# Optimization experiments

Hardware: AMD Instinct MI355X
Metric: run time of the kernel (lower is better)

## Reference

```python
import jax, jax.numpy as jnp
import numpy as np

B, S, OUT = 128, 3000, 84
CODE_SEQ = 30
LAT = 1024
C, D = 128, 16
CB = C * D  # 2048
IN = CODE_SEQ * OUT  # 2520


def setup_inputs() -> dict:
    key = jax.random.key(0)
    ks = jax.random.split(key, 16)
    def w(k, shape):
        fan_in = shape[0]
        return (jax.random.normal(k, shape, dtype=jnp.float32) / np.sqrt(fan_in)).astype(jnp.float32)
    return {
        "y": jax.random.normal(ks[0], (B, S, OUT), dtype=jnp.float32),
        "emb": jax.random.uniform(ks[1], (C, D), minval=-1.0 / C, maxval=1.0 / C, dtype=jnp.float32),
        "eW1": w(ks[2], (IN, LAT)), "eb1": jnp.zeros((LAT,), jnp.float32),
        "eW2": w(ks[3], (LAT, LAT)), "eb2": jnp.zeros((LAT,), jnp.float32),
        "eW3": w(ks[4], (LAT, CB)), "eb3": jnp.zeros((CB,), jnp.float32),
        "dW1": w(ks[5], (CB, LAT)), "db1": jnp.zeros((LAT,), jnp.float32),
        "dW2": w(ks[6], (LAT, LAT)), "db2": jnp.zeros((LAT,), jnp.float32),
        "dW3": w(ks[7], (LAT, IN)), "db3": jnp.zeros((IN,), jnp.float32),
    }


def _mlp(z, W1, b1, W2, b2, W3, b3):
    # LinearEncoder in eval mode (dropout = identity): Linear->ELU->Linear->ELU->Linear
    z = jax.nn.elu(z @ W1 + b1)
    z = jax.nn.elu(z @ W2 + b2)
    return z @ W3 + b3


def reference(y, emb, eW1, eb1, eW2, eb2, eW3, eb3, dW1, db1, dW2, db2, dW3, db3):
    batch, seq_len = y.shape[0], y.shape[1]
    # seq_len % code_seq == 0 -> padding branch is a no-op
    y2 = y.reshape(batch, -1, IN)                 # (B, n_m, 2520)
    n_m = y2.shape[1]
    ze = _mlp(y2, eW1, eb1, eW2, eb2, eW3, eb3)   # (B, n_m, 2048)
    zef = ze.reshape(batch, n_m, -1, D)           # (B, n_m, G=128, 16)
    # squared L2 distance to each of C codes, without materializing (B,n_m,G,C,D)
    dist = (
        jnp.sum(zef ** 2, -1, keepdims=True)
        - 2.0 * jnp.einsum("bngd,cd->bngc", zef, emb)
        + jnp.sum(emb ** 2, -1)
    )                                             # (B, n_m, G, C)
    nn_idx = jnp.argmin(dist, -1)                 # (B, n_m, G)
    zq = emb[nn_idx].reshape(batch, n_m, -1)      # (B, n_m, 2048)
    dec_in = ze + jax.lax.stop_gradient(zq - ze)  # straight-through
    out = _mlp(dec_in, dW1, db1, dW2, db2, dW3, db3)
    out = out.reshape(batch, -1, OUT)[:, :seq_len, :]
    return (out, ze, zq)
```

## Files before the change

kernel.cpp:

```cpp
#include <hip/hip_runtime.h>
#include <hip/hip_bf16.h>
#include <cstdint>
#include <cstddef>

typedef __bf16 bf16_t;
typedef bf16_t bf16x8 __attribute__((ext_vector_type(8)));
typedef float  f32x4  __attribute__((ext_vector_type(4)));

__device__ __forceinline__ void gl_lds16(const void* g, void* l) {
  __builtin_amdgcn_global_load_lds(
      (const __attribute__((address_space(1))) void*)g,
      (__attribute__((address_space(3))) void*)l, 16, 0, 0);
}

#define BAR()  __builtin_amdgcn_s_barrier()
#define LGK0() asm volatile("s_waitcnt lgkmcnt(0)" ::: "memory")

__device__ __forceinline__ void transpose_tile(
    const float* __restrict__ W, bf16_t* __restrict__ Wt,
    int K, int N, int Kpad, int Npad, int bx, int by, int t)
{
  __shared__ float tile[32][33];
  const int tx = t & 31, ty = t >> 5;
  const int k0 = bx * 32, n0 = by * 32;
#pragma unroll
  for (int i = 0; i < 4; ++i) {
    int k = k0 + ty + i * 8, n = n0 + tx;
    tile[ty + i * 8][tx] = (k < K && n < N) ? W[(size_t)k * N + n] : 0.f;
  }
  __syncthreads();
#pragma unroll
  for (int i = 0; i < 4; ++i) {
    int n = n0 + ty + i * 8, k = k0 + tx;
    if (n < Npad && k < Kpad)
      Wt[(size_t)n * Kpad + k] = (bf16_t)tile[tx][ty + i * 8];
  }
}

__global__ __launch_bounds__(256) void prep_kernel(
    const float* __restrict__ y, bf16_t* __restrict__ X0,
    const float* __restrict__ eW1, bf16_t* __restrict__ W1t,
    const float* __restrict__ eW2, bf16_t* __restrict__ W2t,
    const float* __restrict__ eW3, bf16_t* __restrict__ W3t,
    const float* __restrict__ dW1, bf16_t* __restrict__ V1t,
    const float* __restrict__ dW2, bf16_t* __restrict__ V2t,
    const float* __restrict__ dW3, bf16_t* __restrict__ V3t)
{
  const int b = blockIdx.x;
  const int t = threadIdx.x;
  if (b < 16000) {
    const int idx = b * 256 + t;
    const int r = idx / 320, c = (idx % 320) * 8;
    bf16x8 v;
    if (c < 2520) {
      const float4 f0 = *(const float4*)(y + (size_t)r * 2520 + c);
      const float4 f1 = *(const float4*)(y + (size_t)r * 2520 + c + 4);
      v[0] = (bf16_t)f0.x; v[1] = (bf16_t)f0.y; v[2] = (bf16_t)f0.z; v[3] = (bf16_t)f0.w;
      v[4] = (bf16_t)f1.x; v[5] = (bf16_t)f1.y; v[6] = (bf16_t)f1.z; v[7] = (bf16_t)f1.w;
    } else {
#pragma unroll
      for (int j = 0; j < 8; ++j) v[j] = (bf16_t)0.f;
    }
    *(bf16x8*)(X0 + (size_t)r * 2560 + c) = v;
    return;
  }
  int lb = b - 16000;
  if (lb < 2560)      { transpose_tile(eW1, W1t, 2520, 1024, 2560, 1024, lb % 80, lb / 80, t); return; }
  lb -= 2560;
  if (lb < 1024)      { transpose_tile(eW2, W2t, 1024, 1024, 1024, 1024, lb % 32, lb / 32, t); return; }
  lb -= 1024;
  if (lb < 2048)      { transpose_tile(eW3, W3t, 1024, 2048, 1024, 2048, lb % 32, lb / 32, t); return; }
  lb -= 2048;
  if (lb < 2048)      { transpose_tile(dW1, V1t, 2048, 1024, 2048, 1024, lb % 64, lb / 64, t); return; }
  lb -= 2048;
  if (lb < 1024)      { transpose_tile(dW2, V2t, 1024, 1024, 1024, 1024, lb % 32, lb / 32, t); return; }
  lb -= 1024;
  transpose_tile(dW3, V3t, 1024, 2520, 1024, 2560, lb % 32, lb / 32, t);
}

template<int ELU>
__global__ __launch_bounds__(512, 2) void gemm256(
    const bf16_t* __restrict__ A, const bf16_t* __restrict__ Bt,
    const float* __restrict__ bias,
    bf16_t* __restrict__ Cb, float* __restrict__ Cf,
    int M, int N, int K, int Nlog)
{
  __shared__ __align__(16) bf16_t lds[65536];

  const int t  = threadIdx.x;
  const int w  = t >> 6, l = t & 63;
  const int fr = l & 15, kg = l >> 4;
  const int wm = (w >> 2) * 128, wn = (w & 3) * 64;

  const int gx = gridDim.x;
  const int nwg = gx * (int)gridDim.y;
  int lin = blockIdx.y * gx + blockIdx.x;
  int q8 = nwg >> 3, r8 = nwg & 7, xcd = lin & 7, idx = lin >> 3;
  int swz = (xcd < r8 ? xcd * (q8 + 1) : r8 * (q8 + 1) + (xcd - r8) * q8) + idx;
  const int tn = (swz % gx) * 256;
  const int tm = (swz / gx) * 256;

  const int srow = t >> 2;
  const int scol = (t & 3) * 8;
  const int sdst = t * 8;

  const int NT = K >> 5;

  f32x4 acc[8][4];
#pragma unroll
  for (int i = 0; i < 8; ++i)
#pragma unroll
    for (int j = 0; j < 4; ++j) acc[i][j] = (f32x4){0.f, 0.f, 0.f, 0.f};

  auto stageA = [&](int slot, int kn) {
    bf16_t* d = lds + slot * 16384;
    gl_lds16(A + (size_t)(tm + srow) * K + kn + scol,       d + sdst);
    gl_lds16(A + (size_t)(tm + 128 + srow) * K + kn + scol, d + 4096 + sdst);
  };
  auto stageB = [&](int slot, int kn) {
    bf16_t* d = lds + slot * 16384 + 8192;
    gl_lds16(Bt + (size_t)(tn + srow) * K + kn + scol,       d + sdst);
    gl_lds16(Bt + (size_t)(tn + 128 + srow) * K + kn + scol, d + 4096 + sdst);
  };

  stageA(0, 0);  stageB(0, 0);
  stageA(1, 32); stageB(1, 32);
  stageA(2, 64); stageB(2, 64);
  asm volatile("s_waitcnt vmcnt(8)" ::: "memory");
  BAR();

  for (int kt = 0; kt < NT; ++kt) {
    const int slot = kt & 3;
    const bf16_t* aH = lds + slot * 16384 + wm * 32;
    const bf16_t* bH = lds + slot * 16384 + 8192 + wn * 32;
    const bool pf = (kt + 3 < NT);
    const int ps = (kt + 3) & 3;
    const int kn = (kt + 3) << 5;

    bf16x8 af[8], bf_[2];

#pragma unroll
    for (int mi = 0; mi < 8; ++mi)
      af[mi] = *(const bf16x8*)(aH + (mi * 16 + fr) * 32 + kg * 8);
#pragma unroll
    for (int nj = 0; nj < 2; ++nj)
      bf_[nj] = *(const bf16x8*)(bH + (nj * 16 + fr) * 32 + kg * 8);
    if (pf) stageA(ps, kn);
    BAR(); LGK0();
    __builtin_amdgcn_s_setprio(1);
#pragma unroll
    for (int mi = 0; mi < 8; ++mi)
#pragma unroll
      for (int nj = 0; nj < 2; ++nj)
        acc[mi][nj] = __builtin_amdgcn_mfma_f32_16x16x32_bf16(af[mi], bf_[nj], acc[mi][nj], 0, 0, 0);
    __builtin_amdgcn_s_setprio(0);
    BAR();

#pragma unroll
    for (int nj = 0; nj < 2; ++nj)
      bf_[nj] = *(const bf16x8*)(bH + ((nj + 2) * 16 + fr) * 32 + kg * 8);
    if (pf) stageB(ps, kn);
    BAR(); LGK0();
    __builtin_amdgcn_s_setprio(1);
#pragma unroll
    for (int mi = 0; mi < 8; ++mi)
#pragma unroll
      for (int nj = 0; nj < 2; ++nj)
        acc[mi][nj + 2] = __builtin_amdgcn_mfma_f32_16x16x32_bf16(af[mi], bf_[nj], acc[mi][nj + 2], 0, 0, 0);
    __builtin_amdgcn_s_setprio(0);
    asm volatile("s_waitcnt vmcnt(8)" ::: "memory");
    BAR();
  }

#pragma unroll
  for (int mi = 0; mi < 8; ++mi) {
    const int row0 = tm + wm + mi * 16 + kg * 4;
#pragma unroll
    for (int nj = 0; nj < 4; ++nj) {
      const int col = tn + wn + nj * 16 + fr;
      const float bv = (col < Nlog) ? bias[col] : 0.f;
#pragma unroll
      for (int r = 0; r < 4; ++r) {
        float v = acc[mi][nj][r] + bv;
        if (ELU) v = (v > 0.f) ? v : expm1f(v);
        const int row = row0 + r;
        if (Cb) Cb[(size_t)row * N + col] = (bf16_t)v;
        if (Cf && col < Nlog) Cf[(size_t)row * Nlog + col] = v;
      }
    }
  }
}

__global__ __launch_bounds__(256) void vq_mfma(
    const float* __restrict__ ze, const float* __restrict__ emb,
    float* __restrict__ zq, bf16_t* __restrict__ zqb)
{
  __shared__ float  se[2048];
  __shared__ bf16_t seb[2048];
  const int t = threadIdx.x;
  for (int i = t; i < 2048; i += 256) { float v = emb[i]; se[i] = v; seb[i] = (bf16_t)v; }
  __syncthreads();

  const int l = t & 63, w = t >> 6;
  const int col = l & 15;
  const int ks8 = (l >> 4) * 8;
  const bool kact = (ks8 < 16);

  bf16x8 bfrag[8];
  float  hv[8];
#pragma unroll
  for (int cb = 0; cb < 8; ++cb) {
    float s = 0.f;
    bf16x8 bf;
#pragma unroll
    for (int j = 0; j < 8; ++j) bf[j] = (bf16_t)0.f;
    if (kact) {
      const float* ep = se + (cb * 16 + col) * 16 + ks8;
      float4 e0 = *(const float4*)ep;
      float4 e1 = *(const float4*)(ep + 4);
      bf[0] = (bf16_t)e0.x; bf[1] = (bf16_t)e0.y; bf[2] = (bf16_t)e0.z; bf[3] = (bf16_t)e0.w;
      bf[4] = (bf16_t)e1.x; bf[5] = (bf16_t)e1.y; bf[6] = (bf16_t)e1.z; bf[7] = (bf16_t)e1.w;
      s = e0.x*e0.x + e0.y*e0.y + e0.z*e0.z + e0.w*e0.w
        + e1.x*e1.x + e1.y*e1.y + e1.z*e1.z + e1.w*e1.w;
    }
    s += __shfl_xor(s, 16);
    s += __shfl_xor(s, 32);
    bfrag[cb] = bf;
    hv[cb] = 0.5f * s;
  }

  const int base_tile = blockIdx.x * 64 + w * 16;
  for (int it = 0; it < 16; ++it) {
    const int tile = base_tile + it;
    const int row = tile >> 3, g0 = (tile & 7) * 16;

    bf16x8 afrag;
#pragma unroll
    for (int j = 0; j < 8; ++j) afrag[j] = (bf16_t)0.f;
    if (kact) {
      const float* ap = ze + (size_t)row * 2048 + (g0 + col) * 16 + ks8;
      float4 a0 = *(const float4*)ap;
      float4 a1 = *(const float4*)(ap + 4);
      afrag[0] = (bf16_t)(-a0.x); afrag[1] = (bf16_t)(-a0.y);
      afrag[2] = (bf16_t)(-a0.z); afrag[3] = (bf16_t)(-a0.w);
      afrag[4] = (bf16_t)(-a1.x); afrag[5] = (bf16_t)(-a1.y);
      afrag[6] = (bf16_t)(-a1.z); afrag[7] = (bf16_t)(-a1.w);
    }

    f32x4 dd[8];
#pragma unroll
    for (int cb = 0; cb < 8; ++cb) {
      f32x4 c = (f32x4){hv[cb], hv[cb], hv[cb], hv[cb]};
      dd[cb] = __builtin_amdgcn_mfma_f32_16x16x32_bf16(afrag, bfrag[cb], c, 0, 0, 0);
    }

#pragma unroll
    for (int r = 0; r < 4; ++r) {
      float bd = dd[0][r]; int bi = col;
#pragma unroll
      for (int cb = 1; cb < 8; ++cb) {
        float v = dd[cb][r];
        int   ci = cb * 16 + col;
        if (v < bd) { bd = v; bi = ci; }
      }
#pragma unroll
      for (int m = 1; m < 16; m <<= 1) {
        float od = __shfl_xor(bd, m);
        int   oi = __shfl_xor(bi, m);
        if (od < bd || (od == bd && oi < bi)) { bd = od; bi = oi; }
      }
      if (col == r) {
        const int tok = (l >> 4) * 4 + r;
        const size_t go = ((size_t)row * 128 + g0 + tok) * 16;
        const float*  e  = se  + bi * 16;
        const bf16_t* eb = seb + bi * 16;
#pragma unroll
        for (int v = 0; v < 4; ++v)
          *(float4*)(zq + go + v * 4) = ((const float4*)e)[v];
        *(bf16x8*)(zqb + go)     = ((const bf16x8*)eb)[0];
        *(bf16x8*)(zqb + go + 8) = ((const bf16x8*)eb)[1];
      }
    }
  }
}

extern "C" void kernel_launch(void* const* d_in, const int* in_sizes, int n_in,
                              void* d_out, int out_size, void* d_ws, size_t ws_size,
                              hipStream_t stream)
{
  const float* y   = (const float*)d_in[0];
  const float* emb = (const float*)d_in[1];
  const float* eW1 = (const float*)d_in[2];
  const float* eb1 = (const float*)d_in[3];
  const float* eW2 = (const float*)d_in[4];
  const float* eb2 = (const float*)d_in[5];
  const float* eW3 = (const float*)d_in[6];
  const float* eb3 = (const float*)d_in[7];
  const float* dW1 = (const float*)d_in[8];
  const float* db1 = (const float*)d_in[9];
  const float* dW2 = (const float*)d_in[10];
  const float* db2 = (const float*)d_in[11];
  const float* dW3 = (const float*)d_in[12];
  const float* db3 = (const float*)d_in[13];

  float* out = (float*)d_out;
  float* ze  = out + 32256000;
  float* zq  = ze + 26214400;

  uint8_t* ws = (uint8_t*)d_ws;
  size_t off = 0;
  auto alloc = [&](size_t bytes) -> void* {
    void* p = ws + off; off += (bytes + 255) & ~(size_t)255; return p;
  };
  bf16_t* X0  = (bf16_t*)alloc(12800ULL * 2560 * 2);
  bf16_t* W1t = (bf16_t*)alloc(1024ULL * 2560 * 2);
  bf16_t* W2t = (bf16_t*)alloc(1024ULL * 1024 * 2);
  bf16_t* W3t = (bf16_t*)alloc(2048ULL * 1024 * 2);
  bf16_t* V1t = (bf16_t*)alloc(1024ULL * 2048 * 2);
  bf16_t* V2t = (bf16_t*)alloc(1024ULL * 1024 * 2);
  bf16_t* V3t = (bf16_t*)alloc(2560ULL * 1024 * 2);
  bf16_t* H1  = (bf16_t*)alloc(12800ULL * 1024 * 2);
  bf16_t* H2  = (bf16_t*)alloc(12800ULL * 1024 * 2);
  bf16_t* ZQb = (bf16_t*)alloc(12800ULL * 2048 * 2);

  prep_kernel<<<27264, 256, 0, stream>>>(y, X0, eW1, W1t, eW2, W2t, eW3, W3t,
                                         dW1, V1t, dW2, V2t, dW3, V3t);

  gemm256<1><<<dim3(4, 50), 512, 0, stream>>>(X0, W1t, eb1, H1, nullptr, 12800, 1024, 2560, 1024);
  gemm256<1><<<dim3(4, 50), 512, 0, stream>>>(H1, W2t, eb2, H2, nullptr, 12800, 1024, 1024, 1024);
  gemm256<0><<<dim3(8, 50), 512, 0, stream>>>(H2, W3t, eb3, nullptr, ze, 12800, 2048, 1024, 2048);
  vq_mfma<<<1600, 256, 0, stream>>>(ze, emb, zq, ZQb);
  gemm256<1><<<dim3(4, 50), 512, 0, stream>>>(ZQb, V1t, db1, H1, nullptr, 12800, 1024, 2048, 1024);
  gemm256<1><<<dim3(4, 50), 512, 0, stream>>>(H1, V2t, db2, H2, nullptr, 12800, 1024, 1024, 1024);
  gemm256<0><<<dim3(10, 50), 512, 0, stream>>>(H2, V3t, db3, nullptr, out, 12800, 2560, 1024, 2520);
}
```

Before: 662.5 us.

## Fuse all MLP GEMMs and VQ into persistent kernel with dataflow flags

Replaces the six GEMM launches and the VQ launch with one persistent kernel of 256 workgroups. Each workgroup pulls work items from a global atomic counter and waits on per-row-block completion counters before running a tile. This lets later layers start on finished row blocks while earlier layers are still running, removing launch gaps and the idle tail of each 200-tile layer. The cost is atomic polling and spin-waits, two extra hidden-activation buffers, and a dependence on every workgroup being resident at once to avoid deadlock.

```diff
diff --git a/kernel.cpp b/kernel.cpp
--- a/kernel.cpp
+++ b/kernel.cpp
@@ -44,10 +44,14 @@
     const float* __restrict__ eW3, bf16_t* __restrict__ W3t,
     const float* __restrict__ dW1, bf16_t* __restrict__ V1t,
     const float* __restrict__ dW2, bf16_t* __restrict__ V2t,
-    const float* __restrict__ dW3, bf16_t* __restrict__ V3t)
+    const float* __restrict__ dW3, bf16_t* __restrict__ V3t,
+    int* __restrict__ flags)
 {
   const int b = blockIdx.x;
   const int t = threadIdx.x;
+  if (b == 0) {
+    for (int i = t; i < 512; i += 256) flags[i] = 0;
+  }
   if (b < 16000) {
     const int idx = b * 256 + t;
     const int r = idx / 320, c = (idx % 320) * 8;
@@ -78,208 +82,254 @@
   transpose_tile(dW3, V3t, 1024, 2520, 1024, 2560, lb % 32, lb / 32, t);
 }
 
-template<int ELU>
-__global__ __launch_bounds__(512, 2) void gemm256(
-    const bf16_t* __restrict__ A, const bf16_t* __restrict__ Bt,
-    const float* __restrict__ bias,
-    bf16_t* __restrict__ Cb, float* __restrict__ Cf,
-    int M, int N, int K, int Nlog)
+__global__ __launch_bounds__(512, 2) void mega_kernel(
+    const bf16_t* __restrict__ X0,
+    const bf16_t* __restrict__ W1t, const bf16_t* __restrict__ W2t,
+    const bf16_t* __restrict__ W3t, const bf16_t* __restrict__ V1t,
+    const bf16_t* __restrict__ V2t, const bf16_t* __restrict__ V3t,
+    const float* __restrict__ eb1, const float* __restrict__ eb2,
+    const float* __restrict__ eb3, const float* __restrict__ db1,
+    const float* __restrict__ db2, const float* __restrict__ db3,
+    bf16_t* __restrict__ H1, bf16_t* __restrict__ H2,
+    bf16_t* __restrict__ H3, bf16_t* __restrict__ H4,
+    bf16_t* __restrict__ ZQb,
+    float* __restrict__ ze, float* __restrict__ zq, float* __restrict__ outp,
+    const float* __restrict__ emb, int* __restrict__ flags)
 {
-  __shared__ __align__(16) bf16_t lds[65536];
-
-  const int t  = threadIdx.x;
-  const int w  = t >> 6, l = t & 63;
+  __shared__ __align__(16) char smem[131072];
+  __shared__ int s_idx;
+  bf16_t* lds = (bf16_t*)smem;
+
+  const int t = threadIdx.x;
+  const int w = t >> 6, l = t & 63;
   const int fr = l & 15, kg = l >> 4;
-  const int wm = (w >> 2) * 128, wn = (w & 3) * 64;
-
-  const int gx = gridDim.x;
-  const int nwg = gx * (int)gridDim.y;
-  int lin = blockIdx.y * gx + blockIdx.x;
-  int q8 = nwg >> 3, r8 = nwg & 7, xcd = lin & 7, idx = lin >> 3;
-  int swz = (xcd < r8 ? xcd * (q8 + 1) : r8 * (q8 + 1) + (xcd - r8) * q8) + idx;
-  const int tn = (swz % gx) * 256;
-  const int tm = (swz / gx) * 256;
-
-  const int srow = t >> 2;
-  const int scol = (t & 3) * 8;
-  const int sdst = t * 8;
-
-  const int NT = K >> 5;
-
-  f32x4 acc[8][4];
-#pragma unroll
-  for (int i = 0; i < 8; ++i)
-#pragma unroll
-    for (int j = 0; j < 4; ++j) acc[i][j] = (f32x4){0.f, 0.f, 0.f, 0.f};
-
-  auto stageA = [&](int slot, int kn) {
-    bf16_t* d = lds + slot * 16384;
-    gl_lds16(A + (size_t)(tm + srow) * K + kn + scol,       d + sdst);
-    gl_lds16(A + (size_t)(tm + 128 + srow) * K + kn + scol, d + 4096 + sdst);
-  };
-  auto stageB = [&](int slot, int kn) {
-    bf16_t* d = lds + slot * 16384 + 8192;
-    gl_lds16(Bt + (size_t)(tn + srow) * K + kn + scol,       d + sdst);
-    gl_lds16(Bt + (size_t)(tn + 128 + srow) * K + kn + scol, d + 4096 + sdst);
-  };
-
-  stageA(0, 0);  stageB(0, 0);
-  stageA(1, 32); stageB(1, 32);
-  stageA(2, 64); stageB(2, 64);
-  asm volatile("s_waitcnt vmcnt(8)" ::: "memory");
-  BAR();
-
-  for (int kt = 0; kt < NT; ++kt) {
-    const int slot = kt & 3;
-    const bf16_t* aH = lds + slot * 16384 + wm * 32;
-    const bf16_t* bH = lds + slot * 16384 + 8192 + wn * 32;
-    const bool pf = (kt + 3 < NT);
-    const int ps = (kt + 3) & 3;
-    const int kn = (kt + 3) << 5;
-
-    bf16x8 af[8], bf_[2];
-
-#pragma unroll
-    for (int mi = 0; mi < 8; ++mi)
-      af[mi] = *(const bf16x8*)(aH + (mi * 16 + fr) * 32 + kg * 8);
-#pragma unroll
-    for (int nj = 0; nj < 2; ++nj)
-      bf_[nj] = *(const bf16x8*)(bH + (nj * 16 + fr) * 32 + kg * 8);
-    if (pf) stageA(ps, kn);
-    BAR(); LGK0();
-    __builtin_amdgcn_s_setprio(1);
-#pragma unroll
-    for (int mi = 0; mi < 8; ++mi)
-#pragma unroll
-      for (int nj = 0; nj < 2; ++nj)
-        acc[mi][nj] = __builtin_amdgcn_mfma_f32_16x16x32_bf16(af[mi], bf_[nj], acc[mi][nj], 0, 0, 0);
-    __builtin_amdgcn_s_setprio(0);
-    BAR();
-
-#pragma unroll
-    for (int nj = 0; nj < 2; ++nj)
-      bf_[nj] = *(const bf16x8*)(bH + ((nj + 2) * 16 + fr) * 32 + kg * 8);
-    if (pf) stageB(ps, kn);
-    BAR(); LGK0();
-    __builtin_amdgcn_s_setprio(1);
-#pragma unroll
-    for (int mi = 0; mi < 8; ++mi)
-#pragma unroll
-      for (int nj = 0; nj < 2; ++nj)
-        acc[mi][nj + 2] = __builtin_amdgcn_mfma_f32_16x16x32_bf16(af[mi], bf_[nj], acc[mi][nj + 2], 0, 0, 0);
-    __builtin_amdgcn_s_setprio(0);
-    asm volatile("s_waitcnt vmcnt(8)" ::: "memory");
-    BAR();
-  }
-
-#pragma unroll
-  for (int mi = 0; mi < 8; ++mi) {
-    const int row0 = tm + wm + mi * 16 + kg * 4;
-#pragma unroll
-    for (int nj = 0; nj < 4; ++nj) {
-      const int col = tn + wn + nj * 16 + fr;
-      const float bv = (col < Nlog) ? bias[col] : 0.f;
-#pragma unroll
-      for (int r = 0; r < 4; ++r) {
-        float v = acc[mi][nj][r] + bv;
-        if (ELU) v = (v > 0.f) ? v : expm1f(v);
-        const int row = row0 + r;
-        if (Cb) Cb[(size_t)row * N + col] = (bf16_t)v;
-        if (Cf && col < Nlog) Cf[(size_t)row * Nlog + col] = v;
-      }
+
+  for (;;) {
+    if (t == 0)
+      s_idx = __hip_atomic_fetch_add(&flags[0], 1, __ATOMIC_RELAXED, __HIP_MEMORY_SCOPE_AGENT);
+    __syncthreads();
+    const int idx = s_idx;
+    if (idx >= 1900) break;
+
+    int layer, m, n = 0, i = idx;
+    if      (i < 200)  { layer = 0;            m = i >> 2; n = i & 3; }
+    else if (i < 400)  { layer = 1; i -= 200;  m = i >> 2; n = i & 3; }
+    else if (i < 800)  { layer = 2; i -= 400;  m = i >> 3; n = i & 7; }
+    else if (i < 1000) { layer = 3; i -= 800;  m = i; }
+    else if (i < 1200) { layer = 4; i -= 1000; m = i >> 2; n = i & 3; }
+    else if (i < 1400) { layer = 5; i -= 1200; m = i >> 2; n = i & 3; }
+    else               { layer = 6; i -= 1400; m = i / 10; n = i % 10; }
+
+    int depl = -1, need = 0, dm = (layer == 3) ? (m >> 2) : m;
+    if      (layer == 1) { depl = 0; need = 4; }
+    else if (layer == 2) { depl = 1; need = 4; }
+    else if (layer == 3) { depl = 2; need = 8; }
+    else if (layer == 4) { depl = 3; need = 4; }
+    else if (layer == 5) { depl = 4; need = 4; }
+    else if (layer == 6) { depl = 5; need = 4; }
+    if (need) {
+      if (t == 0) {
+        while (__hip_atomic_load(&flags[8 + depl * 64 + dm], __ATOMIC_ACQUIRE,
+                                 __HIP_MEMORY_SCOPE_AGENT) < need)
+          __builtin_amdgcn_s_sleep(2);
+      }
+      __syncthreads();
     }
-  }
-}
-
-__global__ __launch_bounds__(256) void vq_mfma(
-    const float* __restrict__ ze, const float* __restrict__ emb,
-    float* __restrict__ zq, bf16_t* __restrict__ zqb)
-{
-  __shared__ float  se[2048];
-  __shared__ bf16_t seb[2048];
-  const int t = threadIdx.x;
-  for (int i = t; i < 2048; i += 256) { float v = emb[i]; se[i] = v; seb[i] = (bf16_t)v; }
-  __syncthreads();
-
-  const int l = t & 63, w = t >> 6;
-  const int col = l & 15;
-  const int ks8 = (l >> 4) * 8;
-  const bool kact = (ks8 < 16);
-
-  bf16x8 bfrag[8];
-  float  hv[8];
-#pragma unroll
-  for (int cb = 0; cb < 8; ++cb) {
-    float s = 0.f;
-    bf16x8 bf;
-#pragma unroll
-    for (int j = 0; j < 8; ++j) bf[j] = (bf16_t)0.f;
-    if (kact) {
-      const float* ep = se + (cb * 16 + col) * 16 + ks8;
-      float4 e0 = *(const float4*)ep;
-      float4 e1 = *(const float4*)(ep + 4);
-      bf[0] = (bf16_t)e0.x; bf[1] = (bf16_t)e0.y; bf[2] = (bf16_t)e0.z; bf[3] = (bf16_t)e0.w;
-      bf[4] = (bf16_t)e1.x; bf[5] = (bf16_t)e1.y; bf[6] = (bf16_t)e1.z; bf[7] = (bf16_t)e1.w;
-      s = e0.x*e0.x + e0.y*e0.y + e0.z*e0.z + e0.w*e0.w
-        + e1.x*e1.x + e1.y*e1.y + e1.z*e1.z + e1.w*e1.w;
+
+    if (layer != 3) {
+      const bf16_t* A; const bf16_t* Bt; const float* bias;
+      bf16_t* Cb = nullptr; float* Cf = nullptr;
+      int K, Nc, Nlog, elu;
+      switch (layer) {
+        case 0:  A = X0;  Bt = W1t; bias = eb1; Cb = H1; K = 2560; Nc = 1024; Nlog = 1024; elu = 1; break;
+        case 1:  A = H1;  Bt = W2t; bias = eb2; Cb = H2; K = 1024; Nc = 1024; Nlog = 1024; elu = 1; break;
+        case 2:  A = H2;  Bt = W3t; bias = eb3; Cf = ze; K = 1024; Nc = 2048; Nlog = 2048; elu = 0; break;
+        case 4:  A = ZQb; Bt = V1t; bias = db1; Cb = H3; K = 2048; Nc = 1024; Nlog = 1024; elu = 1; break;
+        case 5:  A = H3;  Bt = V2t; bias = db2; Cb = H4; K = 1024; Nc = 1024; Nlog = 1024; elu = 1; break;
+        default: A = H4;  Bt = V3t; bias = db3; Cf = outp; K = 1024; Nc = 2560; Nlog = 2520; elu = 0; break;
+      }
+      const int tm = m * 256, tn = n * 256;
+      const int wm = (w >> 2) * 128, wn = (w & 3) * 64;
+      const int srow = t >> 2, scol = (t & 3) * 8, sdst = t * 8;
+      const int NT = K >> 5;
+
+      f32x4 acc[8][4];
+#pragma unroll
+      for (int a = 0; a < 8; ++a)
+#pragma unroll
+        for (int b = 0; b < 4; ++b) acc[a][b] = (f32x4){0.f, 0.f, 0.f, 0.f};
+
+      auto stageA = [&](int slot, int kn) {
+        bf16_t* d = lds + slot * 16384;
+        gl_lds16(A + (size_t)(tm + srow) * K + kn + scol,       d + sdst);
+        gl_lds16(A + (size_t)(tm + 128 + srow) * K + kn + scol, d + 4096 + sdst);
+      };
+      auto stageB = [&](int slot, int kn) {
+        bf16_t* d = lds + slot * 16384 + 8192;
+        gl_lds16(Bt + (size_t)(tn + srow) * K + kn + scol,       d + sdst);
+        gl_lds16(Bt + (size_t)(tn + 128 + srow) * K + kn + scol, d + 4096 + sdst);
+      };
+
+      stageA(0, 0);  stageB(0, 0);
+      stageA(1, 32); stageB(1, 32);
+      stageA(2, 64); stageB(2, 64);
+      asm volatile("s_waitcnt vmcnt(8)" ::: "memory");
+      BAR();
+
+      for (int kt = 0; kt < NT; ++kt) {
+        const int slot = kt & 3;
+        const bf16_t* aH = lds + slot * 16384 + wm * 32;
+        const bf16_t* bH = lds + slot * 16384 + 8192 + wn * 32;
+        const bool pf = (kt + 3 < NT);
+        const int ps = (kt + 3) & 3;
+        const int kn = (kt + 3) << 5;
+
+        bf16x8 af[8], bf_[2];
+#pragma unroll
+        for (int mi = 0; mi < 8; ++mi)
+          af[mi] = *(const bf16x8*)(aH + (mi * 16 + fr) * 32 + kg * 8);
+#pragma unroll
+        for (int nj = 0; nj < 2; ++nj)
+          bf_[nj] = *(const bf16x8*)(bH + (nj * 16 + fr) * 32 + kg * 8);
+        if (pf) stageA(ps, kn);
+        BAR(); LGK0();
+        __builtin_amdgcn_s_setprio(1);
+#pragma unroll
+        for (int mi = 0; mi < 8; ++mi)
+#pragma unroll
+          for (int nj = 0; nj < 2; ++nj)
+            acc[mi][nj] = __builtin_amdgcn_mfma_f32_16x16x32_bf16(af[mi], bf_[nj], acc[mi][nj], 0, 0, 0);
+        __builtin_amdgcn_s_setprio(0);
+        BAR();
+
+#pragma unroll
+        for (int nj = 0; nj < 2; ++nj)
+          bf_[nj] = *(const bf16x8*)(bH + ((nj + 2) * 16 + fr) * 32 + kg * 8);
+        if (pf) stageB(ps, kn);
+        BAR(); LGK0();
+        __builtin_amdgcn_s_setprio(1);
+#pragma unroll
+        for (int mi = 0; mi < 8; ++mi)
+#pragma unroll
+          for (int nj = 0; nj < 2; ++nj)
+            acc[mi][nj + 2] = __builtin_amdgcn_mfma_f32_16x16x32_bf16(af[mi], bf_[nj], acc[mi][nj + 2], 0, 0, 0);
+        __builtin_amdgcn_s_setprio(0);
+        asm volatile("s_waitcnt vmcnt(8)" ::: "memory");
+        BAR();
+      }
+
+#pragma unroll
+      for (int mi = 0; mi < 8; ++mi) {
+        const int row0 = tm + wm + mi * 16 + kg * 4;
+#pragma unroll
+        for (int nj = 0; nj < 4; ++nj) {
+          const int col = tn + wn + nj * 16 + fr;
+          const float bv = (col < Nlog) ? bias[col] : 0.f;
+#pragma unroll
+          for (int r = 0; r < 4; ++r) {
+            float v = acc[mi][nj][r] + bv;
+            if (elu && v <= 0.f) v = expm1f(v);
+            const int row = row0 + r;
+            if (Cb) Cb[(size_t)row * Nc + col] = (bf16_t)v;
+            if (Cf && col < Nlog) Cf[(size_t)row * Nlog + col] = v;
+          }
+        }
+      }
+    } else {
+      float*  se  = (float*)smem;
+      bf16_t* seb = (bf16_t*)(smem + 8192);
+      for (int q = t; q < 2048; q += 512) { float v = emb[q]; se[q] = v; seb[q] = (bf16_t)v; }
+      __syncthreads();
+
+      const int col = l & 15;
+      const int ks8 = (l >> 4) * 8;
+      const bool kact = (ks8 < 16);
+
+      bf16x8 bfrag[8];
+      float  hv[8];
+#pragma unroll
+      for (int cb = 0; cb < 8; ++cb) {
+        float s = 0.f;
+        bf16x8 bf;
+#pragma unroll
+        for (int j = 0; j < 8; ++j) bf[j] = (bf16_t)0.f;
+        if (kact) {
+          const float* ep = se + (cb * 16 + col) * 16 + ks8;
+          float4 e0 = *(const float4*)ep;
+          float4 e1 = *(const float4*)(ep + 4);
+          bf[0] = (bf16_t)e0.x; bf[1] = (bf16_t)e0.y; bf[2] = (bf16_t)e0.z; bf[3] = (bf16_t)e0.w;
+          bf[4] = (bf16_t)e1.x; bf[5] = (bf16_t)e1.y; bf[6] = (bf16_t)e1.z; bf[7] = (bf16_t)e1.w;
+          s = e0.x*e0.x + e0.y*e0.y + e0.z*e0.z + e0.w*e0.w
+            + e1.x*e1.x + e1.y*e1.y + e1.z*e1.z + e1.w*e1.w;
+        }
+        s += __shfl_xor(s, 16);
+        s += __shfl_xor(s, 32);
+        bfrag[cb] = bf;
+        hv[cb] = 0.5f * s;
+      }
+
+      const int rbase = m * 64;
+      for (int it = 0; it < 64; ++it) {
+        const int wt = w * 64 + it;
+        const int row = rbase + (wt >> 3);
+        const int g0 = (wt & 7) * 16;
+
+        bf16x8 afrag;
+#pragma unroll
+        for (int j = 0; j < 8; ++j) afrag[j] = (bf16_t)0.f;
+        if (kact) {
+          const float* ap = ze + (size_t)row * 2048 + (g0 + col) * 16 + ks8;
+          float4 a0 = *(const float4*)ap;
+          float4 a1 = *(const float4*)(ap + 4);
+          afrag[0] = (bf16_t)(-a0.x); afrag[1] = (bf16_t)(-a0.y);
+          afrag[2] = (bf16_t)(-a0.z); afrag[3] = (bf16_t)(-a0.w);
+          afrag[4] = (bf16_t)(-a1.x); afrag[5] = (bf16_t)(-a1.y);
+          afrag[6] = (bf16_t)(-a1.z); afrag[7] = (bf16_t)(-a1.w);
+        }
+
+        f32x4 dd[8];
+#pragma unroll
+        for (int cb = 0; cb < 8; ++cb) {
+          f32x4 c = (f32x4){hv[cb], hv[cb], hv[cb], hv[cb]};
+          dd[cb] = __builtin_amdgcn_mfma_f32_16x16x32_bf16(afrag, bfrag[cb], c, 0, 0, 0);
+        }
+
+#pragma unroll
+        for (int r = 0; r < 4; ++r) {
+          float bd = dd[0][r]; int bi = col;
+#pragma unroll
+          for (int cb = 1; cb < 8; ++cb) {
+            float v = dd[cb][r];
+            int   ci = cb * 16 + col;
+            if (v < bd) { bd = v; bi = ci; }
+          }
+#pragma unroll
+          for (int mm = 1; mm < 16; mm <<= 1) {
+            float od = __shfl_xor(bd, mm);
+            int   oi = __shfl_xor(bi, mm);
+            if (od < bd || (od == bd && oi < bi)) { bd = od; bi = oi; }
+          }
+          if (col == r) {
+            const int tok = (l >> 4) * 4 + r;
+            const size_t go = ((size_t)row * 128 + g0 + tok) * 16;
+            const float*  e  = se  + bi * 16;
+            const bf16_t* eb = seb + bi * 16;
+#pragma unroll
+            for (int v = 0; v < 4; ++v)
+              *(float4*)(zq + go + v * 4) = ((const float4*)e)[v];
+            *(bf16x8*)(ZQb + go)     = ((const bf16x8*)eb)[0];
+            *(bf16x8*)(ZQb + go + 8) = ((const bf16x8*)eb)[1];
+          }
+        }
+      }
     }
-    s += __shfl_xor(s, 16);
-    s += __shfl_xor(s, 32);
-    bfrag[cb] = bf;
-    hv[cb] = 0.5f * s;
-  }
-
-  const int base_tile = blockIdx.x * 64 + w * 16;
-  for (int it = 0; it < 16; ++it) {
-    const int tile = base_tile + it;
-    const int row = tile >> 3, g0 = (tile & 7) * 16;
-
-    bf16x8 afrag;
-#pragma unroll
-    for (int j = 0; j < 8; ++j) afrag[j] = (bf16_t)0.f;
-    if (kact) {
-      const float* ap = ze + (size_t)row * 2048 + (g0 + col) * 16 + ks8;
-      float4 a0 = *(const float4*)ap;
-      float4 a1 = *(const float4*)(ap + 4);
-      afrag[0] = (bf16_t)(-a0.x); afrag[1] = (bf16_t)(-a0.y);
-      afrag[2] = (bf16_t)(-a0.z); afrag[3] = (bf16_t)(-a0.w);
-      afrag[4] = (bf16_t)(-a1.x); afrag[5] = (bf16_t)(-a1.y);
-      afrag[6] = (bf16_t)(-a1.z); afrag[7] = (bf16_t)(-a1.w);
-    }
-
-    f32x4 dd[8];
-#pragma unroll
-    for (int cb = 0; cb < 8; ++cb) {
-      f32x4 c = (f32x4){hv[cb], hv[cb], hv[cb], hv[cb]};
-      dd[cb] = __builtin_amdgcn_mfma_f32_16x16x32_bf16(afrag, bfrag[cb], c, 0, 0, 0);
-    }
-
-#pragma unroll
-    for (int r = 0; r < 4; ++r) {
-      float bd = dd[0][r]; int bi = col;
-#pragma unroll
-      for (int cb = 1; cb < 8; ++cb) {
-        float v = dd[cb][r];
-        int   ci = cb * 16 + col;
-        if (v < bd) { bd = v; bi = ci; }
-      }
-#pragma unroll
-      for (int m = 1; m < 16; m <<= 1) {
-        float od = __shfl_xor(bd, m);
-        int   oi = __shfl_xor(bi, m);
-        if (od < bd || (od == bd && oi < bi)) { bd = od; bi = oi; }
-      }
-      if (col == r) {
-        const int tok = (l >> 4) * 4 + r;
-        const size_t go = ((size_t)row * 128 + g0 + tok) * 16;
-        const float*  e  = se  + bi * 16;
-        const bf16_t* eb = seb + bi * 16;
-#pragma unroll
-        for (int v = 0; v < 4; ++v)
-          *(float4*)(zq + go + v * 4) = ((const float4*)e)[v];
-        *(bf16x8*)(zqb + go)     = ((const bf16x8*)eb)[0];
-        *(bf16x8*)(zqb + go + 8) = ((const bf16x8*)eb)[1];
-      }
+
+    __threadfence();
+    __syncthreads();
+    if (t == 0 && layer != 6) {
+      const int pm = (layer == 3) ? (m >> 2) : m;
+      __hip_atomic_fetch_add(&flags[8 + layer * 64 + pm], 1, __ATOMIC_RELEASE,
+                             __HIP_MEMORY_SCOPE_AGENT);
     }
   }
 }
@@ -321,16 +371,16 @@
   bf16_t* V3t = (bf16_t*)alloc(2560ULL * 1024 * 2);
   bf16_t* H1  = (bf16_t*)alloc(12800ULL * 1024 * 2);
   bf16_t* H2  = (bf16_t*)alloc(12800ULL * 1024 * 2);
+  bf16_t* H3  = (bf16_t*)alloc(12800ULL * 1024 * 2);
+  bf16_t* H4  = (bf16_t*)alloc(12800ULL * 1024 * 2);
   bf16_t* ZQb = (bf16_t*)alloc(12800ULL * 2048 * 2);
+  int*    flags = (int*)alloc(512 * 4);
 
   prep_kernel<<<27264, 256, 0, stream>>>(y, X0, eW1, W1t, eW2, W2t, eW3, W3t,
-                                         dW1, V1t, dW2, V2t, dW3, V3t);
-
-  gemm256<1><<<dim3(4, 50), 512, 0, stream>>>(X0, W1t, eb1, H1, nullptr, 12800, 1024, 2560, 1024);
-  gemm256<1><<<dim3(4, 50), 512, 0, stream>>>(H1, W2t, eb2, H2, nullptr, 12800, 1024, 1024, 1024);
-  gemm256<0><<<dim3(8, 50), 512, 0, stream>>>(H2, W3t, eb3, nullptr, ze, 12800, 2048, 1024, 2048);
-  vq_mfma<<<1600, 256, 0, stream>>>(ze, emb, zq, ZQb);
-  gemm256<1><<<dim3(4, 50), 512, 0, stream>>>(ZQb, V1t, db1, H1, nullptr, 12800, 1024, 2048, 1024);
-  gemm256<1><<<dim3(4, 50), 512, 0, stream>>>(H1, V2t, db2, H2, nullptr, 12800, 1024, 1024, 1024);
-  gemm256<0><<<dim3(10, 50), 512, 0, stream>>>(H2, V3t, db3, nullptr, out, 12800, 2560, 1024, 2520);
-}
+                                         dW1, V1t, dW2, V2t, dW3, V3t, flags);
+
+  mega_kernel<<<256, 512, 0, stream>>>(X0, W1t, W2t, W3t, V1t, V2t, V3t,
+                                       eb1, eb2, eb3, db1, db2, db3,
+                                       H1, H2, H3, H4, ZQb,
+                                       ze, zq, out, emb, flags);
+}
```

New measurement: 2.260 ms. 3.41x slower.
